# Optimization experiments

Hardware: AMD Instinct MI355X
Metric: run time of the kernel (lower is better)

## Reference

```python
import jax, jax.numpy as jnp
import numpy as np

NUM_HEADS = 16
ROPE_BASE = 10000.0


def _rotate_half(x):
    x1, x2 = jnp.split(x, 2, axis=-1)
    return jnp.concatenate([-x2, x1], axis=-1)


def _rope_cos_sin(seq_len, dim, dtype):
    # GPT-NeoX rotary: inv_freq over even dims, emb = concat(freqs, freqs)
    inv_freq = 1.0 / (ROPE_BASE ** (jnp.arange(0, dim, 2, dtype=jnp.float32) / dim))
    t = jnp.arange(seq_len, dtype=jnp.float32)
    freqs = jnp.einsum('s,d->sd', t, inv_freq)          # [S, dim/2]
    emb = jnp.concatenate([freqs, freqs], axis=-1)       # [S, dim]
    cos = jnp.cos(emb).astype(dtype)[:, None, None, :]   # [S,1,1,dim]
    sin = jnp.sin(emb).astype(dtype)[:, None, None, :]
    return cos, sin


def setup_inputs() -> dict:
    key = jax.random.key(0)
    k1, k2, k3 = jax.random.split(key, 3)
    S, B, H = 2048, 2, 2048
    x = jax.random.normal(k1, (S, B, H), dtype=jnp.float32)
    w_qkv = jax.random.normal(k2, (H, 3 * H), dtype=jnp.float32) * 0.02
    w_dense = jax.random.normal(k3, (H, H), dtype=jnp.float32) * 0.02
    return {"x": x, "w_qkv": w_qkv, "w_dense": w_dense}


def reference(x, w_qkv, w_dense):
    # x: [S, B, H] (Megatron seq-first layout)
    S, B, H = x.shape
    hd = H // NUM_HEADS

    qkv = jnp.einsum('sbh,hk->sbk', x, w_qkv)                  # fused QKV proj
    qkv = qkv.reshape(S, B, NUM_HEADS, 3 * hd)
    q, k, v = jnp.split(qkv, 3, axis=-1)                       # each [S,B,nh,hd]

    cos, sin = _rope_cos_sin(S, hd, x.dtype)
    q = q * cos + _rotate_half(q) * sin
    k = k * cos + _rotate_half(k) * sin

    norm_factor = jnp.asarray(np.sqrt(hd), dtype=x.dtype)
    scores = jnp.einsum('sbhd,tbhd->bhst', q, k) / norm_factor  # [B,nh,S,S]

    # causal mask (attention_mask_func fills masked with large negative)
    causal = jnp.tril(jnp.ones((S, S), dtype=bool))
    scores = jnp.where(causal, scores, jnp.asarray(-1e4, dtype=scores.dtype))

    # softmax in fp32 (attention_softmax_in_fp32)
    probs = jax.nn.softmax(scores.astype(jnp.float32), axis=-1).astype(x.dtype)

    ctx = jnp.einsum('bhst,tbhd->sbhd', probs, v).reshape(S, B, H)
    out = jnp.einsum('sbh,hk->sbk', ctx, w_dense)               # row-parallel dense (skip_bias_add)
    return out
```

## Files before the change

### kernel.cpp

```cpp
#include <hip/hip_runtime.h>
#include <cstdint>
#include <cstddef>

typedef _Float16 v8h __attribute__((ext_vector_type(8)));
typedef _Float16 v4h __attribute__((ext_vector_type(4)));
typedef _Float16 v2h __attribute__((ext_vector_type(2)));
typedef float v4f __attribute__((ext_vector_type(4)));
typedef float v16f __attribute__((ext_vector_type(16)));

#define NH 16
#define HD 128
#define SLEN 2048
#define BATCH 2
#define HID 2048

__device__ __forceinline__ void gload16(const void* gptr, void* lptr) {
  __builtin_amdgcn_global_load_lds(
      (const __attribute__((address_space(1))) unsigned int*)gptr,
      (__attribute__((address_space(3))) unsigned int*)lptr, 16, 0, 0);
}

__device__ __forceinline__ uint32_t pkh(float a, float b) {
  return __builtin_bit_cast(uint32_t, __builtin_amdgcn_cvt_pkrtz(a, b));
}
__device__ __forceinline__ v2h pkh2(float a, float b) {
  return __builtin_bit_cast(v2h, __builtin_amdgcn_cvt_pkrtz(a, b));
}
__device__ __forceinline__ uint32_t xswap32(uint32_t x) {
  return (uint32_t)__shfl_xor((int)x, 32, 64);
}


__global__ __launch_bounds__(256) void cast_x_kernel(const float* __restrict__ in,
                                                     _Float16* __restrict__ out, int n4) {
  int i = blockIdx.x * 256 + threadIdx.x;
  if (i >= n4) return;
  const float4 v = ((const float4*)in)[i];
  v4h o; o[0] = (_Float16)v.x; o[1] = (_Float16)v.y; o[2] = (_Float16)v.z; o[3] = (_Float16)v.w;
  *(v4h*)(out + (size_t)i * 4) = o;
}

__global__ __launch_bounds__(256) void transpose_cast_kernel(const float* __restrict__ W,
                                                             _Float16* __restrict__ WT,
                                                             int R, int C) {
  __shared__ float tl[64][65];
  int tx = threadIdx.x, ty = threadIdx.y;
  int c0 = blockIdx.x * 64, r0 = blockIdx.y * 64;
#pragma unroll
  for (int i = 0; i < 8; ++i) {
    int r = ty + i * 8;
#pragma unroll
    for (int j = 0; j < 2; ++j) {
      int c = tx + j * 32;
      tl[c][r] = W[(size_t)(r0 + r) * C + c0 + c];
    }
  }
  __syncthreads();
#pragma unroll
  for (int i = 0; i < 8; ++i) {
    int c = ty + i * 8;
    v2h o; o[0] = (_Float16)tl[c][2 * tx]; o[1] = (_Float16)tl[c][2 * tx + 1];
    *(v2h*)(WT + (size_t)(c0 + c) * R + r0 + 2 * tx) = o;
  }
}

__global__ void rope_table_kernel(float2* __restrict__ csl) {
  int s = blockIdx.x, i = threadIdx.x;
  float inv = powf(10000.0f, -(float)i * (1.0f / 64.0f));
  float ang = (float)s * inv;
  csl[s * 64 + i] = make_float2(cosf(ang), sinf(ang));
}

template <int MODE>
__global__ __launch_bounds__(256) void gemm_kernel(const _Float16* __restrict__ A,
                                                   const _Float16* __restrict__ BT,
                                                   int M, int N, int K, int gy,
                                                   _Float16* __restrict__ q_out,
                                                   _Float16* __restrict__ k_out,
                                                   _Float16* __restrict__ vt_out,
                                                   float* __restrict__ f_out,
                                                   const float2* __restrict__ csl) {
  __shared__ alignas(16) char As[2][16384];
  __shared__ alignas(16) char Bs[2][16384];
  const int t = threadIdx.x;
  const int w = t >> 6;
  const int l = t & 63;
  const int wr = w >> 1, wc = w & 1;

  const int total = gridDim.x;
  const int F = blockIdx.x;
  const int gid = (F & 7) * (total >> 3) + (F >> 3);
  const int bx = gid / gy, by = gid % gy;
  const int m0 = by * 128;
  const int n0 = bx * 128;

  const char* aS[4];
  const char* bS[4];
  {
    const int Kb = K * 2;
#pragma unroll
    for (int j = 0; j < 4; ++j) {
      int c = w * 256 + j * 64 + l;
      int row = c >> 3;
      int col = ((c & 7) * 16) ^ ((row & 7) << 4);
      aS[j] = (const char*)A + (size_t)(m0 + row) * Kb + col;
      bS[j] = (const char*)BT + (size_t)(n0 + row) * Kb + col;
    }
  }

  const v4f vzero = {0.f, 0.f, 0.f, 0.f};
  v4f acc[4][4];
#pragma unroll
  for (int mi = 0; mi < 4; ++mi)
#pragma unroll
    for (int ni = 0; ni < 4; ++ni) acc[mi][ni] = vzero;

  auto stage = [&](int ks, int d) {
#pragma unroll
    for (int j = 0; j < 4; ++j) {
      gload16(aS[j] + ks * 128, &As[d][w * 4096 + j * 1024]);
      gload16(bS[j] + ks * 128, &Bs[d][w * 4096 + j * 1024]);
    }
  };

  const int nk = K >> 6;
  stage(0, 0);
  for (int ks = 0; ks < nk; ++ks) {
    asm volatile("s_waitcnt vmcnt(0)" ::: "memory");
    __syncthreads();
    if (ks + 1 < nk) stage(ks + 1, (ks + 1) & 1);
    const char* Ap = As[ks & 1];
    const char* Bp = Bs[ks & 1];
#pragma unroll
    for (int kk = 0; kk < 2; ++kk) {
      v8h a[4], b[4];
#pragma unroll
      for (int mi = 0; mi < 4; ++mi) {
        int row = wr * 64 + mi * 16 + (l & 15);
        a[mi] = *(const v8h*)(Ap + row * 128 + ((kk * 64 + ((l >> 4) * 16)) ^ ((row & 7) << 4)));
      }
#pragma unroll
      for (int ni = 0; ni < 4; ++ni) {
        int row = wc * 64 + ni * 16 + (l & 15);
        b[ni] = *(const v8h*)(Bp + row * 128 + ((kk * 64 + ((l >> 4) * 16)) ^ ((row & 7) << 4)));
      }
      __builtin_amdgcn_s_setprio(1);
#pragma unroll
      for (int mi = 0; mi < 4; ++mi)
#pragma unroll
        for (int ni = 0; ni < 4; ++ni)
          acc[mi][ni] = __builtin_amdgcn_mfma_f32_16x16x32_f16(a[mi], b[ni], acc[mi][ni], 0, 0, 0);
      __builtin_amdgcn_s_setprio(0);
    }
  }

  if (MODE == 1) {
#pragma unroll
    for (int mi = 0; mi < 4; ++mi)
#pragma unroll
      for (int ni = 0; ni < 4; ++ni) {
        int n = n0 + wc * 64 + ni * 16 + (l & 15);
#pragma unroll
        for (int r = 0; r < 4; ++r) {
          int m = m0 + wr * 64 + mi * 16 + (l >> 4) * 4 + r;
          f_out[(size_t)m * N + n] = acc[mi][ni][r];
        }
      }
  } else {
    const int bt = bx % 3;
    const int head = bx / 3;
    const int l15 = l & 15;
    const int h4 = (l >> 4) * 4;
    if (bt == 2) {
      _Float16* vb = (_Float16*)&As[0][0];
      __syncthreads();
#pragma unroll
      for (int mi = 0; mi < 4; ++mi)
#pragma unroll
        for (int ni = 0; ni < 4; ++ni) {
          int d = wc * 64 + ni * 16 + l15;
#pragma unroll
          for (int r = 0; r < 4; ++r) {
            int mm = wr * 64 + mi * 16 + h4 + r;
            vb[d * 128 + (mm ^ ((d & 15) << 2))] = (_Float16)acc[mi][ni][r];
          }
        }
      __syncthreads();
      const int s0 = m0 >> 1;
      for (int i = 0; i < 64; ++i) {
        int row = w * 64 + i;
        int d = row >> 1, b = row & 1;
        int mm = 2 * l + b;
        _Float16 val = vb[d * 128 + (mm ^ ((d & 15) << 2))];
        vt_out[(((size_t)(b * NH + head)) * HD + d) * SLEN + s0 + l] = val;
      }
    } else {
      _Float16* dst = (bt == 0) ? q_out : k_out;
      float* xb2 = (w < 2) ? (float*)As + (size_t)w * 4096
                           : (float*)Bs + (size_t)(w - 2) * 4096;
      float* pb2 = ((w ^ 1) < 2) ? (float*)As + (size_t)(w ^ 1) * 4096
                                 : (float*)Bs + (size_t)((w ^ 1) - 2) * 4096;
      __syncthreads();
#pragma unroll
      for (int mi = 0; mi < 4; ++mi)
#pragma unroll
        for (int ni = 0; ni < 4; ++ni)
#pragma unroll
          for (int r = 0; r < 4; ++r) {
            int row = h4 + r;
            xb2[(mi * 4 + ni) * 256 + row * 16 + (l15 ^ row)] = acc[mi][ni][r];
          }
      __syncthreads();
      const float sgn = (wc == 0) ? -1.f : 1.f;
#pragma unroll
      for (int mi = 0; mi < 4; ++mi) {
#pragma unroll
        for (int ni = 0; ni < 4; ++ni) {
          int dd = ni * 16 + l15;
          int d = wc * 64 + dd;
#pragma unroll
          for (int r = 0; r < 4; ++r) {
            int row = h4 + r;
            int m = m0 + wr * 64 + mi * 16 + row;
            int s = m >> 1;
            float partner = pb2[(mi * 4 + ni) * 256 + row * 16 + (l15 ^ row)];
            const float2 cs = csl[s * 64 + dd];
            float val = acc[mi][ni][r] * cs.x + sgn * partner * cs.y;
            dst[(((size_t)((m & 1) * NH + head)) * SLEN + s) * HD + d] = (_Float16)val;
          }
        }
      }
    }
  }
}

__global__ __launch_bounds__(256, 2) void attn_kernel(const _Float16* __restrict__ Qb,
                                                      const _Float16* __restrict__ Kb,
                                                      const _Float16* __restrict__ VTb,
                                                      _Float16* __restrict__ ctx) {
  __shared__ alignas(16) char Ks[2][16384];
  __shared__ alignas(16) char Vs[2][16384];
  const int t = threadIdx.x;
  const int w = t >> 6;
  const int l = t & 63;
  const int F = blockIdx.x;
  const int bh = (F & 7) + 8 * ((F >> 3) & 3);
  const int pr = F >> 5;
  const int ta = pr, tb = 31 - pr;
  const int grp = w >> 1;
  const int tile = grp ? tb : ta;
  const int q0 = tile * 64 + (w & 1) * 32;
  const int l31 = l & 31, g = l >> 5;
  const int q = q0 + l31;

  const _Float16* Qp = Qb + (size_t)bh * SLEN * HD;
  const _Float16* Kp = Kb + (size_t)bh * SLEN * HD;
  const _Float16* Vp = VTb + (size_t)bh * HD * SLEN;

  const char* kS[4];
  const char* vS[4];
#pragma unroll
  for (int j = 0; j < 4; ++j) {
    int c = w * 256 + j * 64 + l;
    {
      int row = c >> 4;
      int col = ((c & 15) * 16) ^ ((row & 7) << 4);
      kS[j] = (const char*)Kp + (size_t)row * 256 + col;
    }
    {
      int row = c >> 3;
      int col = ((c & 7) * 16) ^ ((row & 7) << 4);
      vS[j] = (const char*)Vp + (size_t)row * (SLEN * 2) + col;
    }
  }
  auto stage = [&](int kt, int d) {
#pragma unroll
    for (int j = 0; j < 4; ++j) {
      gload16(kS[j] + (size_t)kt * 16384, &Ks[d][w * 4096 + j * 1024]);
      gload16(vS[j] + (size_t)kt * 128, &Vs[d][w * 4096 + j * 1024]);
    }
  };

  v8h qf[8];
#pragma unroll
  for (int c = 0; c < 8; ++c)
    qf[c] = *(const v8h*)(Qp + (size_t)q * HD + c * 16 + g * 8);

  v16f oT[4];
#pragma unroll
  for (int dc = 0; dc < 4; ++dc)
#pragma unroll
    for (int r = 0; r < 16; ++r) oT[dc][r] = 0.f;
  float m_run = -1e30f, l_run = 0.f;
  const float scale = 0.08838834764831845f;

  stage(0, 0);
  for (int kt = 0; kt <= tb; ++kt) {
    asm volatile("s_waitcnt vmcnt(0)" ::: "memory");
    __syncthreads();
    if (kt < tb) stage(kt + 1, (kt + 1) & 1);
    if (grp == 0 && kt > ta) continue;
    const char* Kst = Ks[kt & 1];
    const char* Vst = Vs[kt & 1];

    v16f s0, s1;
#pragma unroll
    for (int r = 0; r < 16; ++r) { s0[r] = 0.f; s1[r] = 0.f; }
    __builtin_amdgcn_s_setprio(1);
#pragma unroll
    for (int c = 0; c < 8; ++c) {
      int cofs = (c * 32 + g * 16);
      v8h kf0 = *(const v8h*)(Kst + l31 * 256 + (cofs ^ ((l31 & 7) << 4)));
      v8h kf1 = *(const v8h*)(Kst + (32 + l31) * 256 + (cofs ^ ((l31 & 7) << 4)));
      s0 = __builtin_amdgcn_mfma_f32_32x32x16_f16(kf0, qf[c], s0, 0, 0, 0);
      s1 = __builtin_amdgcn_mfma_f32_32x32x16_f16(kf1, qf[c], s1, 0, 0, 0);
    }
    __builtin_amdgcn_s_setprio(0);

    const bool diag = (kt == tile);
    const int kv0 = kt * 64;
    float pv[32];
#pragma unroll
    for (int r = 0; r < 16; ++r) {
      int kofs = (r & 3) + 8 * (r >> 2) + 4 * g;
      float a = s0[r] * scale;
      float b = s1[r] * scale;
      if (diag) {
        if (kv0 + kofs > q) a = -1e4f;
        if (kv0 + 32 + kofs > q) b = -1e4f;
      }
      pv[r] = a;
      pv[16 + r] = b;
    }

    float mx[8];
#pragma unroll
    for (int i = 0; i < 8; ++i)
      mx[i] = fmaxf(fmaxf(pv[i], pv[i + 8]), fmaxf(pv[i + 16], pv[i + 24]));
    float pm = fmaxf(fmaxf(fmaxf(mx[0], mx[1]), fmaxf(mx[2], mx[3])),
                     fmaxf(fmaxf(mx[4], mx[5]), fmaxf(mx[6], mx[7])));
    float pmall = fmaxf(pm, __shfl_xor(pm, 32, 64));

    float mnew;
    if (__all(pmall - m_run <= 8.f)) {
      mnew = m_run;
    } else {
      mnew = fmaxf(m_run, pmall);
      float alpha = __expf(m_run - mnew);
      m_run = mnew;
      l_run *= alpha;
#pragma unroll
      for (int dc = 0; dc < 4; ++dc)
#pragma unroll
        for (int r = 0; r < 16; ++r) oT[dc][r] *= alpha;
    }

    float sacc0 = 0.f, sacc1 = 0.f, sacc2 = 0.f, sacc3 = 0.f;
#pragma unroll
    for (int i = 0; i < 8; ++i) { pv[i] = __expf(pv[i] - mnew); sacc0 += pv[i]; }
#pragma unroll
    for (int i = 8; i < 16; ++i) { pv[i] = __expf(pv[i] - mnew); sacc1 += pv[i]; }
#pragma unroll
    for (int i = 16; i < 24; ++i) { pv[i] = __expf(pv[i] - mnew); sacc2 += pv[i]; }
#pragma unroll
    for (int i = 24; i < 32; ++i) { pv[i] = __expf(pv[i] - mnew); sacc3 += pv[i]; }
    float ssum = (sacc0 + sacc1) + (sacc2 + sacc3);
    l_run += ssum + __shfl_xor(ssum, 32, 64);

    __builtin_amdgcn_s_setprio(1);
#pragma unroll
    for (int c = 0; c < 4; ++c) {
      int base = (c >> 1) * 16 + (c & 1) * 8;
      uint32_t P0 = pkh(pv[base + 0], pv[base + 1]);
      uint32_t P1 = pkh(pv[base + 2], pv[base + 3]);
      uint32_t P2 = pkh(pv[base + 4], pv[base + 5]);
      uint32_t P3 = pkh(pv[base + 6], pv[base + 7]);
      uint32_t T0 = g ? P0 : P2;
      uint32_t T1 = g ? P1 : P3;
      uint32_t U0 = xswap32(T0);
      uint32_t U1 = xswap32(T1);
      union { uint32_t u[4]; v8h h; } pu;
      pu.u[0] = g ? U0 : P0;
      pu.u[1] = g ? U1 : P1;
      pu.u[2] = g ? P2 : U0;
      pu.u[3] = g ? P3 : U1;
      v8h pf = pu.h;
      int cofs = c * 32 + g * 16;
#pragma unroll
      for (int dc = 0; dc < 4; ++dc) {
        int vrow = dc * 32 + l31;
        v8h vf = *(const v8h*)(Vst + vrow * 128 + (cofs ^ ((vrow & 7) << 4)));
        oT[dc] = __builtin_amdgcn_mfma_f32_32x32x16_f16(vf, pf, oT[dc], 0, 0, 0);
      }
    }
    __builtin_amdgcn_s_setprio(0);
  }

  const float inv = 1.0f / l_run;
  const int b = bh >> 4;
  const int hh = bh & 15;
  _Float16* orow = ctx + ((size_t)q * BATCH + b) * HID + hh * HD;
#pragma unroll
  for (int dc = 0; dc < 4; ++dc) {
#pragma unroll
    for (int rr = 0; rr < 4; ++rr) {
      v2h w0 = pkh2(oT[dc][4 * rr + 0] * inv, oT[dc][4 * rr + 1] * inv);
      v2h w1 = pkh2(oT[dc][4 * rr + 2] * inv, oT[dc][4 * rr + 3] * inv);
      v4h o4; o4[0] = w0[0]; o4[1] = w0[1]; o4[2] = w1[0]; o4[3] = w1[1];
      *(v4h*)(orow + dc * 32 + rr * 8 + g * 4) = o4;
    }
  }
}


extern "C" void kernel_launch(void* const* d_in, const int* in_sizes, int n_in,
                              void* d_out, int out_size, void* d_ws, size_t ws_size,
                              hipStream_t stream) {
  const float* x = (const float*)d_in[0];
  const float* w_qkv = (const float*)d_in[1];
  const float* w_dense = (const float*)d_in[2];
  float* out = (float*)d_out;
  char* ws = (char*)d_ws;

  _Float16* xb    = (_Float16*)(ws);
  _Float16* wqkvT = (_Float16*)(ws + 16777216);
  _Float16* wdT   = (_Float16*)(ws + 41943040);
  _Float16* Qb    = (_Float16*)(ws + 50331648);
  _Float16* Kb    = (_Float16*)(ws + 67108864);
  _Float16* VTb   = (_Float16*)(ws + 100663296);
  _Float16* ctx   = (_Float16*)(ws + 117440512);
  float2* csl     = (float2*)(ws + 134217728);

  cast_x_kernel<<<dim3(8192), dim3(256), 0, stream>>>(x, xb, 2097152);
  transpose_cast_kernel<<<dim3(96, 32), dim3(32, 8), 0, stream>>>(w_qkv, wqkvT, 2048, 6144);
  transpose_cast_kernel<<<dim3(32, 32), dim3(32, 8), 0, stream>>>(w_dense, wdT, 2048, 2048);
  rope_table_kernel<<<dim3(2048), dim3(64), 0, stream>>>(csl);

  gemm_kernel<0><<<dim3(1536), dim3(256), 0, stream>>>(xb, wqkvT, 4096, 6144, 2048, 32,
                                                       Qb, Kb, VTb, (float*)nullptr, csl);
  attn_kernel<<<dim3(512), dim3(256), 0, stream>>>(Qb, Kb, VTb, ctx);
  gemm_kernel<1><<<dim3(512), dim3(256), 0, stream>>>(ctx, wdT, 4096, 2048, 2048, 32,
                                                      (_Float16*)nullptr, (_Float16*)nullptr,
                                                      (_Float16*)nullptr, out,
                                                      (const float2*)nullptr);
}
```

Baseline: 268.8 us.

## Read K and V fragments directly from global memory instead of LDS staging

Removes the double-buffered LDS staging of K and V tiles, along with its async global-to-LDS loads and per-iteration barriers. Each wave now loads its MFMA operand fragments straight from global memory and iterates only up to its own causal tile. This drops the shared-memory footprint and the block-wide synchronization. The cost is redundant global/L2 traffic across waves, since K and V are no longer shared through LDS, and there is no software prefetch to hide load latency.

```diff
diff --git a/kernel.cpp b/kernel.cpp
--- a/kernel.cpp
+++ b/kernel.cpp
@@ -238,8 +238,6 @@
                                                       const _Float16* __restrict__ Kb,
                                                       const _Float16* __restrict__ VTb,
                                                       _Float16* __restrict__ ctx) {
-  __shared__ alignas(16) char Ks[2][16384];
-  __shared__ alignas(16) char Vs[2][16384];
   const int t = threadIdx.x;
   const int w = t >> 6;
   const int l = t & 63;
@@ -257,30 +255,6 @@
   const _Float16* Kp = Kb + (size_t)bh * SLEN * HD;
   const _Float16* Vp = VTb + (size_t)bh * HD * SLEN;
 
-  const char* kS[4];
-  const char* vS[4];
-#pragma unroll
-  for (int j = 0; j < 4; ++j) {
-    int c = w * 256 + j * 64 + l;
-    {
-      int row = c >> 4;
-      int col = ((c & 15) * 16) ^ ((row & 7) << 4);
-      kS[j] = (const char*)Kp + (size_t)row * 256 + col;
-    }
-    {
-      int row = c >> 3;
-      int col = ((c & 7) * 16) ^ ((row & 7) << 4);
-      vS[j] = (const char*)Vp + (size_t)row * (SLEN * 2) + col;
-    }
-  }
-  auto stage = [&](int kt, int d) {
-#pragma unroll
-    for (int j = 0; j < 4; ++j) {
-      gload16(kS[j] + (size_t)kt * 16384, &Ks[d][w * 4096 + j * 1024]);
-      gload16(vS[j] + (size_t)kt * 128, &Vs[d][w * 4096 + j * 1024]);
-    }
-  };
-
   v8h qf[8];
 #pragma unroll
   for (int c = 0; c < 8; ++c)
@@ -294,14 +268,9 @@
   float m_run = -1e30f, l_run = 0.f;
   const float scale = 0.08838834764831845f;
 
-  stage(0, 0);
-  for (int kt = 0; kt <= tb; ++kt) {
-    asm volatile("s_waitcnt vmcnt(0)" ::: "memory");
-    __syncthreads();
-    if (kt < tb) stage(kt + 1, (kt + 1) & 1);
-    if (grp == 0 && kt > ta) continue;
-    const char* Kst = Ks[kt & 1];
-    const char* Vst = Vs[kt & 1];
+  const int nkt = tile + 1;
+  for (int kt = 0; kt < nkt; ++kt) {
+    const int kv0 = kt * 64;
 
     v16f s0, s1;
 #pragma unroll
@@ -309,16 +278,14 @@
     __builtin_amdgcn_s_setprio(1);
 #pragma unroll
     for (int c = 0; c < 8; ++c) {
-      int cofs = (c * 32 + g * 16);
-      v8h kf0 = *(const v8h*)(Kst + l31 * 256 + (cofs ^ ((l31 & 7) << 4)));
-      v8h kf1 = *(const v8h*)(Kst + (32 + l31) * 256 + (cofs ^ ((l31 & 7) << 4)));
+      v8h kf0 = *(const v8h*)(Kp + (size_t)(kv0 + l31) * HD + c * 16 + g * 8);
+      v8h kf1 = *(const v8h*)(Kp + (size_t)(kv0 + 32 + l31) * HD + c * 16 + g * 8);
       s0 = __builtin_amdgcn_mfma_f32_32x32x16_f16(kf0, qf[c], s0, 0, 0, 0);
       s1 = __builtin_amdgcn_mfma_f32_32x32x16_f16(kf1, qf[c], s1, 0, 0, 0);
     }
     __builtin_amdgcn_s_setprio(0);
 
     const bool diag = (kt == tile);
-    const int kv0 = kt * 64;
     float pv[32];
 #pragma unroll
     for (int r = 0; r < 16; ++r) {
@@ -385,11 +352,9 @@
       pu.u[2] = g ? P2 : U0;
       pu.u[3] = g ? P3 : U1;
       v8h pf = pu.h;
-      int cofs = c * 32 + g * 16;
 #pragma unroll
       for (int dc = 0; dc < 4; ++dc) {
-        int vrow = dc * 32 + l31;
-        v8h vf = *(const v8h*)(Vst + vrow * 128 + (cofs ^ ((vrow & 7) << 4)));
+        v8h vf = *(const v8h*)(Vp + (size_t)(dc * 32 + l31) * SLEN + kv0 + c * 16 + g * 8);
         oT[dc] = __builtin_amdgcn_mfma_f32_32x32x16_f16(vf, pf, oT[dc], 0, 0, 0);
       }
     }
```

After: 345.9 us. +28.7%, slower.
